# Kernel optimization log

Hardware: AMD Instinct MI355X
Metric: run time of the kernel (lower is better)

The kernel has to match this reference:

```python
import jax, jax.numpy as jnp
import numpy as np

B, N, FIN, FOUT, E = 2, 50000, 128, 64, 800000


def setup_inputs() -> dict:
    key = jax.random.key(0)
    ks = jax.random.split(key, 7)
    x = jax.random.normal(ks[0], (B, N, FIN), dtype=jnp.float32)
    W = jax.random.normal(ks[1], (FIN, FOUT), dtype=jnp.float32) * (1.0 / np.sqrt(FIN))
    W_self = jax.random.normal(ks[2], (FIN, FOUT), dtype=jnp.float32) * (1.0 / np.sqrt(FIN))
    b_self = jax.random.normal(ks[3], (FOUT,), dtype=jnp.float32) * 0.01
    edge_row = jax.random.randint(ks[4], (E,), 0, N, dtype=jnp.int32)
    edge_col = jax.random.randint(ks[5], (E,), 0, N, dtype=jnp.int32)
    edge_val = jax.random.uniform(ks[6], (E,), dtype=jnp.float32)
    return {"x": x, "W": W, "W_self": W_self, "b_self": b_self,
            "edge_row": edge_row, "edge_col": edge_col, "edge_val": edge_val}


def reference(x, W, W_self, b_self, edge_row, edge_col, edge_val):
    # x: (B, N, FIN); adjacency in COO form: out[r] += val * in[c]
    Bn, Nn, _ = x.shape
    Fo = W.shape[1]
    x_trans = jnp.einsum("bnf,fo->bno", x, W)               # (B, N, FOUT), no bias
    # Same layout trick as torch: sparse.mm over (N, B*FOUT)
    xr = x_trans.transpose(1, 0, 2).reshape(Nn, Bn * Fo)    # (N, B*FOUT)
    msgs = edge_val[:, None] * xr[edge_col]                  # (E, B*FOUT) gather
    agg = jax.ops.segment_sum(msgs, edge_row, num_segments=Nn)  # (N, B*FOUT) scatter-add
    agg = agg.reshape(Nn, Bn, Fo).transpose(1, 0, 2)         # (B, N, FOUT)
    self_c = jnp.einsum("bnf,fo->bno", x, W_self) + b_self   # Linear with bias
    return jax.nn.relu(self_c + agg)
```

## Files before the change

kernel.cpp:

```cpp
#include <hip/hip_runtime.h>
#include <hip/hip_fp16.h>

#define Bc   2
#define Nn   50000
#define FINc 128
#define FOUTc 64
#define Mtot (Bc * Nn)
#define CCOMB 128
#define GB 1563
#define CB 782

typedef __bf16 bf16x8 __attribute__((ext_vector_type(8)));
typedef float  f32x4  __attribute__((ext_vector_type(4)));

static __device__ inline unsigned short f2bf(float f) {
    unsigned int u = __float_as_uint(f);
    u += 0x7fffu + ((u >> 16) & 1u);
    return (unsigned short)(u >> 16);
}

__global__ __launch_bounds__(256) void pack_w(
    const float* __restrict__ W, const float* __restrict__ Ws,
    unsigned short* __restrict__ Bp)
{
    const int idx = blockIdx.x * 256 + threadIdx.x;
    const int lane = idx & 63;
    const int kt   = (idx >> 6) & 3;
    const int nt   = idx >> 8;
    const int n    = nt * 16 + (lane & 15);
    const int k0   = kt * 32 + (lane >> 4) * 8;
    unsigned short o8[8];
#pragma unroll
    for (int j = 0; j < 8; ++j) {
        const int f = k0 + j;
        const float v = (n < 64) ? W[f * FOUTc + n] : Ws[f * FOUTc + (n - 64)];
        o8[j] = f2bf(v);
    }
    *(uint4*)&Bp[(size_t)idx * 8] = *(uint4*)o8;
}

__global__ __launch_bounds__(256) void gemm_count(
    const float* __restrict__ x, const unsigned short* __restrict__ Bp,
    const float* __restrict__ bself,
    unsigned short* __restrict__ xrb, float* __restrict__ outp,
    const int* __restrict__ erow, int* __restrict__ cntp,
    int* __restrict__ rank, int E)
{
    if (blockIdx.x >= GB) {
        const int base = (blockIdx.x - GB) * 1024 + threadIdx.x * 4;
        if (base + 4 <= E) {
            const int4 r4 = *(const int4*)&erow[base];
            const int k0 = atomicAdd(&cntp[(size_t)r4.x * 16], 1);
            const int k1 = atomicAdd(&cntp[(size_t)r4.y * 16], 1);
            const int k2 = atomicAdd(&cntp[(size_t)r4.z * 16], 1);
            const int k3 = atomicAdd(&cntp[(size_t)r4.w * 16], 1);
            *(int4*)&rank[base] = make_int4(k0, k1, k2, k3);
        }
        return;
    }

    const int wave = threadIdx.x >> 6;
    const int lane = threadIdx.x & 63;
    const int quad = lane >> 4;
    const int mbase = blockIdx.x * 64 + wave * 16;

    const int mrow   = mbase + (lane & 15);
    const int mclamp = (mrow < Mtot) ? mrow : (Mtot - 1);
    const float* __restrict__ xrow = &x[(size_t)mclamp * FINc];

    f32x4 acc[8] = {};

#pragma unroll
    for (int kt = 0; kt < 4; ++kt) {
        const int k0 = kt * 32 + quad * 8;
        const float4 xa = *(const float4*)&xrow[k0];
        const float4 xb = *(const float4*)&xrow[k0 + 4];
        bf16x8 bf;
        bf[0] = (__bf16)xa.x; bf[1] = (__bf16)xa.y;
        bf[2] = (__bf16)xa.z; bf[3] = (__bf16)xa.w;
        bf[4] = (__bf16)xb.x; bf[5] = (__bf16)xb.y;
        bf[6] = (__bf16)xb.z; bf[7] = (__bf16)xb.w;

        const bf16x8* __restrict__ abase =
            (const bf16x8*)&Bp[(size_t)(kt * 64 + lane) * 8];
#pragma unroll
        for (int nt = 0; nt < 8; ++nt) {
            const bf16x8 af = abase[nt * 4 * 64];
            acc[nt] = __builtin_amdgcn_mfma_f32_16x16x32_bf16(af, bf, acc[nt], 0, 0, 0);
        }
    }

    const int m = mbase + (lane & 15);
    if (m < Mtot) {
        const int b = (m >= Nn) ? 1 : 0;
        const int n = m - b * Nn;
        unsigned short* __restrict__ xp = &xrb[(size_t)n * CCOMB + b * FOUTc];
        const int cq = quad * 4;
#pragma unroll
        for (int nt = 0; nt < 4; ++nt) {
            const int c = nt * 16 + cq;
            unsigned short h[4];
            h[0] = f2bf(acc[nt][0]); h[1] = f2bf(acc[nt][1]);
            h[2] = f2bf(acc[nt][2]); h[3] = f2bf(acc[nt][3]);
            *(uint2*)&xp[c] = *(uint2*)h;
        }
        float* __restrict__ op = &outp[(size_t)m * FOUTc];
#pragma unroll
        for (int nt = 4; nt < 8; ++nt) {
            const int o = (nt - 4) * 16 + cq;
            const float4 b4 = *(const float4*)&bself[o];
            float4 v;
            v.x = acc[nt][0] + b4.x; v.y = acc[nt][1] + b4.y;
            v.z = acc[nt][2] + b4.z; v.w = acc[nt][3] + b4.w;
            *(float4*)&op[o] = v;
        }
    }
}

__global__ __launch_bounds__(256) void block_sum(
    const int* __restrict__ cntp, int* __restrict__ bsum)
{
    __shared__ int s[256];
    const int t = threadIdx.x;
    const int idx = blockIdx.x * 256 + t;
    s[t] = (idx < Nn) ? cntp[(size_t)idx * 16] : 0;
    __syncthreads();
    for (int off = 128; off > 0; off >>= 1) {
        if (t < off) s[t] += s[t + off];
        __syncthreads();
    }
    if (t == 0) bsum[blockIdx.x] = s[0];
}

__global__ __launch_bounds__(256) void scan_bsum(
    const int* __restrict__ bsum, int* __restrict__ bscan, int nb)
{
    __shared__ int s[256];
    const int t = threadIdx.x;
    const int v = (t < nb) ? bsum[t] : 0;
    s[t] = v;
    __syncthreads();
    for (int off = 1; off < 256; off <<= 1) {
        const int add = (t >= off) ? s[t - off] : 0;
        __syncthreads();
        s[t] += add;
        __syncthreads();
    }
    if (t < nb) bscan[t] = s[t] - v;
}

__global__ __launch_bounds__(256) void fill_starts(
    const int* __restrict__ cntp, const int* __restrict__ bscan,
    int* __restrict__ rowstart, int E)
{
    __shared__ int s[256];
    const int t = threadIdx.x;
    const int idx = blockIdx.x * 256 + t;
    const int v = (idx < Nn) ? cntp[(size_t)idx * 16] : 0;
    s[t] = v;
    __syncthreads();
    for (int off = 1; off < 256; off <<= 1) {
        const int add = (t >= off) ? s[t - off] : 0;
        __syncthreads();
        s[t] += add;
        __syncthreads();
    }
    if (idx < Nn) rowstart[idx] = bscan[blockIdx.x] + (s[t] - v);
    if (idx == 0) rowstart[Nn] = E;
}

__global__ __launch_bounds__(256) void bucket(
    const int* __restrict__ erow, const int* __restrict__ ecol,
    const float* __restrict__ evalv, const int* __restrict__ rank,
    const int* __restrict__ rowstart, unsigned int* __restrict__ cvp, int E)
{
    const int e = blockIdx.x * 512 + threadIdx.x * 2;
    if (e + 2 > E) return;
    const int2   r2 = *(const int2*)&erow[e];
    const int2   c2 = *(const int2*)&ecol[e];
    const float2 v2 = *(const float2*)&evalv[e];
    const int2   k2 = *(const int2*)&rank[e];
    const unsigned int h0 = __half_as_ushort(__float2half(v2.x));
    const unsigned int h1 = __half_as_ushort(__float2half(v2.y));
    cvp[rowstart[r2.x] + k2.x] = (h0 << 17) | (unsigned int)c2.x;
    cvp[rowstart[r2.y] + k2.y] = (h1 << 17) | (unsigned int)c2.y;
}

#define GATH16(EIDX, ACC)                                                     \
    {                                                                         \
        const unsigned int w = cvp[EIDX];                                     \
        const float vv = __half2float(__ushort_as_half(                       \
                             (unsigned short)(w >> 17)));                     \
        const uint4 raw = *(const uint4*)&xrb[(size_t)(w & 0x1FFFFu) * CCOMB + c0]; \
        ACC[0] = fmaf(vv, __uint_as_float(raw.x << 16),         ACC[0]);      \
        ACC[1] = fmaf(vv, __uint_as_float(raw.x & 0xffff0000u), ACC[1]);      \
        ACC[2] = fmaf(vv, __uint_as_float(raw.y << 16),         ACC[2]);      \
        ACC[3] = fmaf(vv, __uint_as_float(raw.y & 0xffff0000u), ACC[3]);      \
        ACC[4] = fmaf(vv, __uint_as_float(raw.z << 16),         ACC[4]);      \
        ACC[5] = fmaf(vv, __uint_as_float(raw.z & 0xffff0000u), ACC[5]);      \
        ACC[6] = fmaf(vv, __uint_as_float(raw.w << 16),         ACC[6]);      \
        ACC[7] = fmaf(vv, __uint_as_float(raw.w & 0xffff0000u), ACC[7]);      \
    }

__global__ __launch_bounds__(256) void row_gather(
    const int* __restrict__ rowstart, const unsigned int* __restrict__ cvp,
    const unsigned short* __restrict__ xrb, float* __restrict__ outp)
{
    const int lane = threadIdx.x & 63;
    int n = blockIdx.x * 4 + (threadIdx.x >> 6);
    n = __builtin_amdgcn_readfirstlane(n);

    const int s    = rowstart[n];
    const int eend = rowstart[n + 1];
    const int sub  = lane >> 4;
    const int c0   = (lane & 15) * 8;

    float aA[8] = {0.f, 0.f, 0.f, 0.f, 0.f, 0.f, 0.f, 0.f};
    float aB[8] = {0.f, 0.f, 0.f, 0.f, 0.f, 0.f, 0.f, 0.f};

    int e = s;
    for (; e + 8 <= eend; e += 8) {
        GATH16(e + sub,     aA);
        GATH16(e + 4 + sub, aB);
    }
    for (; e < eend; e += 4) {
        if (e + sub < eend) GATH16(e + sub, aA);
    }

#pragma unroll
    for (int i = 0; i < 8; ++i) {
        aA[i] += aB[i];
        aA[i] += __shfl_down(aA[i], 16);
        aA[i] += __shfl_down(aA[i], 32);
    }

    if (lane < 16) {
        const int b = c0 >> 6;
        const int o = c0 & 63;
        const size_t oidx = ((size_t)b * Nn + n) * FOUTc + o;
        float4 s0 = *(float4*)&outp[oidx];
        float4 s1 = *(float4*)&outp[oidx + 4];
        s0.x = fmaxf(s0.x + aA[0], 0.0f);
        s0.y = fmaxf(s0.y + aA[1], 0.0f);
        s0.z = fmaxf(s0.z + aA[2], 0.0f);
        s0.w = fmaxf(s0.w + aA[3], 0.0f);
        s1.x = fmaxf(s1.x + aA[4], 0.0f);
        s1.y = fmaxf(s1.y + aA[5], 0.0f);
        s1.z = fmaxf(s1.z + aA[6], 0.0f);
        s1.w = fmaxf(s1.w + aA[7], 0.0f);
        *(float4*)&outp[oidx]     = s0;
        *(float4*)&outp[oidx + 4] = s1;
    }
}

extern "C" void kernel_launch(void* const* d_in, const int* in_sizes, int n_in,
                              void* d_out, int out_size, void* d_ws, size_t ws_size,
                              hipStream_t stream)
{
    const float* x    = (const float*)d_in[0];
    const float* W    = (const float*)d_in[1];
    const float* Ws   = (const float*)d_in[2];
    const float* bs   = (const float*)d_in[3];
    const int*   erow = (const int*)d_in[4];
    const int*   ecol = (const int*)d_in[5];
    const float* eval = (const float*)d_in[6];
    float* outp = (float*)d_out;
    const int E = in_sizes[4];

    unsigned short* xrb = (unsigned short*)d_ws;
    unsigned int* cvp = (unsigned int*)(xrb + (size_t)Nn * CCOMB);
    int* rank     = (int*)(cvp + E);
    int* rowstart = rank + E;
    int* cntp     = rowstart + (Nn + 4);
    int* bsum     = cntp + (size_t)Nn * 16;
    int* bscan    = bsum + 256;
    unsigned short* Bp = (unsigned short*)(bscan + 256);

    const int NB = (Nn + 255) / 256;

    hipMemsetAsync(cntp, 0, (size_t)Nn * 16 * sizeof(int), stream);
    pack_w<<<8, 256, 0, stream>>>(W, Ws, Bp);

    gemm_count<<<GB + CB, 256, 0, stream>>>(x, Bp, bs, xrb, outp,
                                            erow, cntp, rank, E);

    block_sum<<<NB, 256, 0, stream>>>(cntp, bsum);
    scan_bsum<<<1, 256, 0, stream>>>(bsum, bscan, NB);
    fill_starts<<<NB, 256, 0, stream>>>(cntp, bscan, rowstart, E);

    bucket<<<(E + 511) / 512, 256, 0, stream>>>(erow, ecol, eval, rank,
                                                rowstart, cvp, E);

    row_gather<<<Nn / 4, 256, 0, stream>>>(rowstart, cvp, xrb, outp);
}
```

Measured before the change: 209.0 us.

## Stage packed weights in LDS, run count blocks first, widen gather unroll

The GEMM blocks now copy the packed bf16 weight matrix (32 KB) into shared memory and feed the MFMA operands from LDS instead of global/L2. Block order is swapped so the atomic edge-counting blocks get dispatched before the GEMM blocks. The row gather kernel uses four independent accumulators and 16-edge strides to keep more loads in flight. In exchange, the 32 KB of LDS per block may limit GEMM occupancy, and the extra accumulators raise register use in the gather.

```diff
diff --git a/kernel.cpp b/kernel.cpp
--- a/kernel.cpp
+++ b/kernel.cpp
@@ -46,8 +46,10 @@
     const int* __restrict__ erow, int* __restrict__ cntp,
     int* __restrict__ rank, int E)
 {
-    if (blockIdx.x >= GB) {
-        const int base = (blockIdx.x - GB) * 1024 + threadIdx.x * 4;
+    __shared__ unsigned short BpL[2048 * 8];
+
+    if (blockIdx.x < CB) {
+        const int base = blockIdx.x * 1024 + threadIdx.x * 4;
         if (base + 4 <= E) {
             const int4 r4 = *(const int4*)&erow[base];
             const int k0 = atomicAdd(&cntp[(size_t)r4.x * 16], 1);
@@ -59,10 +61,14 @@
         return;
     }
 
-    const int wave = threadIdx.x >> 6;
+#pragma unroll
+    for (int i = 0; i < 8; ++i)
+        ((uint4*)BpL)[i * 256 + threadIdx.x] = ((const uint4*)Bp)[i * 256 + threadIdx.x];
+    __syncthreads();
+
     const int lane = threadIdx.x & 63;
     const int quad = lane >> 4;
-    const int mbase = blockIdx.x * 64 + wave * 16;
+    const int mbase = (blockIdx.x - CB) * 64 + (threadIdx.x >> 6) * 16;
 
     const int mrow   = mbase + (lane & 15);
     const int mclamp = (mrow < Mtot) ? mrow : (Mtot - 1);
@@ -81,11 +87,9 @@
         bf[4] = (__bf16)xb.x; bf[5] = (__bf16)xb.y;
         bf[6] = (__bf16)xb.z; bf[7] = (__bf16)xb.w;
 
-        const bf16x8* __restrict__ abase =
-            (const bf16x8*)&Bp[(size_t)(kt * 64 + lane) * 8];
 #pragma unroll
         for (int nt = 0; nt < 8; ++nt) {
-            const bf16x8 af = abase[nt * 4 * 64];
+            const bf16x8 af = *(const bf16x8*)&BpL[(size_t)((nt * 4 + kt) * 64 + lane) * 8];
             acc[nt] = __builtin_amdgcn_mfma_f32_16x16x32_bf16(af, bf, acc[nt], 0, 0, 0);
         }
     }
@@ -217,19 +221,30 @@
 
     float aA[8] = {0.f, 0.f, 0.f, 0.f, 0.f, 0.f, 0.f, 0.f};
     float aB[8] = {0.f, 0.f, 0.f, 0.f, 0.f, 0.f, 0.f, 0.f};
+    float aC[8] = {0.f, 0.f, 0.f, 0.f, 0.f, 0.f, 0.f, 0.f};
+    float aD[8] = {0.f, 0.f, 0.f, 0.f, 0.f, 0.f, 0.f, 0.f};
 
     int e = s;
-    for (; e + 8 <= eend; e += 8) {
+    for (; e + 16 <= eend; e += 16) {
+        GATH16(e + sub,      aA);
+        GATH16(e + 4 + sub,  aB);
+        GATH16(e + 8 + sub,  aC);
+        GATH16(e + 12 + sub, aD);
+    }
+    if (e + 8 <= eend) {
         GATH16(e + sub,     aA);
         GATH16(e + 4 + sub, aB);
+        e += 8;
     }
     for (; e < eend; e += 4) {
-        if (e + sub < eend) GATH16(e + sub, aA);
+        if (e + sub < eend) GATH16(e + sub, aC);
     }
 
 #pragma unroll
     for (int i = 0; i < 8; ++i) {
         aA[i] += aB[i];
+        aC[i] += aD[i];
+        aA[i] += aC[i];
         aA[i] += __shfl_down(aA[i], 16);
         aA[i] += __shfl_down(aA[i], 32);
     }
@@ -281,7 +296,7 @@
     hipMemsetAsync(cntp, 0, (size_t)Nn * 16 * sizeof(int), stream);
     pack_w<<<8, 256, 0, stream>>>(W, Ws, Bp);
 
-    gemm_count<<<GB + CB, 256, 0, stream>>>(x, Bp, bs, xrb, outp,
+    gemm_count<<<CB + GB, 256, 0, stream>>>(x, Bp, bs, xrb, outp,
                                             erow, cntp, rank, E);
 
     block_sum<<<NB, 256, 0, stream>>>(cntp, bsum);
```

New measurement: 208.4 us. About the same (-0.3%).
